# Performance work log

Hardware: AMD Instinct MI355X
Metric: run time of the kernel (lower is better)

## Reference

```python
import jax, jax.numpy as jnp
import numpy as np

B, N, D4 = 64, 2048, 4

def setup_inputs() -> dict:
    key = jax.random.key(0)
    k1, k2 = jax.random.split(key)
    p = jax.random.normal(k1, (B, N, D4), dtype=jnp.float32)
    q = jax.random.normal(k2, (B, N, D4), dtype=jnp.float32)
    return {"p": p, "q": q}

def reference(p, q):
    # loss_norm_choice='p3', im=False, take_sqrt=True, jet_features=False
    p3 = p[..., 1:]  # (B, N, 3) spatial momenta
    q3 = q[..., 1:]
    p_sq = jnp.sum(p3 * p3, axis=-1)                      # (B, N)
    q_sq = jnp.sum(q3 * q3, axis=-1)                      # (B, N)
    cross = jnp.einsum('bnd,bmd->bnm', p3, q3)            # (B, N, N)
    dist_sq = p_sq[:, :, None] + q_sq[:, None, :] - 2.0 * cross
    dist = jnp.sqrt(jnp.maximum(dist_sq, 0.0) + 1e-16)    # (B, N, N)
    min_pq = jnp.min(dist, axis=-1)                       # (B, N) nearest q for each p
    min_qp = jnp.min(dist, axis=-2)                       # (B, N) nearest p for each q
    return jnp.sum((min_pq + min_qp) * 0.5)
```

## Files before the change

kernel.cpp:

```cpp
#include <hip/hip_runtime.h>
#include <math.h>


typedef _Float16 half8 __attribute__((ext_vector_type(8)));
typedef float floatx16 __attribute__((ext_vector_type(16)));

constexpr int B_ = 64;
constexpr int N_ = 2048;
constexpr int NT = N_ / 32;
constexpr int BLOCK = 512;
constexpr int WPB = 8;
constexpr int BFRAGS = 2;
constexpr int IBLK = NT / (WPB * BFRAGS);
constexpr int NBLK = IBLK * B_ * 2;

__global__ __launch_bounds__(BLOCK, 4) void chamfer_mfma_kernel(
    const float* __restrict__ p, const float* __restrict__ q,
    float* __restrict__ partials)
{
    __shared__ half8 Aarr[NT * 64];
    __shared__ float wsum[WPB];

    const int dir = blockIdx.z;
    const int b   = blockIdx.y;
    const float4* rowsA = (const float4*)((dir == 0 ? q : p) + (size_t)b * N_ * 4);
    const float4* colsB = (const float4*)((dir == 0 ? p : q) + (size_t)b * N_ * 4);

    for (int j = threadIdx.x; j < N_; j += BLOCK) {
        float4 v = rowsA[j];
        _Float16 x = (_Float16)v.y, y = (_Float16)v.z, z = (_Float16)v.w;
        float xf = (float)x, yf = (float)y, zf = (float)z;
        float sq = fmaf(xf, xf, fmaf(yf, yf, zf * zf));
        half8 lo;
        lo[0] = x; lo[1] = y; lo[2] = z; lo[3] = (_Float16)1.0f;
        lo[4] = (_Float16)(-0.5f * sq);
        lo[5] = (_Float16)0.0f; lo[6] = (_Float16)0.0f; lo[7] = (_Float16)0.0f;
        half8 zero8;
#pragma unroll
        for (int e = 0; e < 8; ++e) zero8[e] = (_Float16)0.0f;
        const int tile = j >> 5, r = j & 31;
        Aarr[tile * 64 + r]      = lo;
        Aarr[tile * 64 + 32 + r] = zero8;
    }

    const int lane = threadIdx.x & 63;
    const int wid  = threadIdx.x >> 6;
    const int W    = blockIdx.x * WPB + wid;
    half8 bf[BFRAGS];
#pragma unroll
    for (int t = 0; t < BFRAGS; ++t) {
        float4 v = colsB[(W * BFRAGS + t) * 32 + (lane & 31)];
        _Float16 x = (_Float16)v.y, y = (_Float16)v.z, z = (_Float16)v.w;
        float xf = (float)x, yf = (float)y, zf = (float)z;
        float sq = fmaf(xf, xf, fmaf(yf, yf, zf * zf));
#pragma unroll
        for (int e = 0; e < 8; ++e) bf[t][e] = (_Float16)0.0f;
        if (lane < 32) {
            bf[t][0] = x; bf[t][1] = y; bf[t][2] = z;
            bf[t][3] = (_Float16)(-0.5f * sq);
            bf[t][4] = (_Float16)1.0f;
        }
    }
    __syncthreads();

    floatx16 zero;
#pragma unroll
    for (int i = 0; i < 16; ++i) zero[i] = 0.0f;

    float cmx0 = -3.4e38f, cmx1 = -3.4e38f;
#pragma unroll 4
    for (int J = 0; J < NT; ++J) {
        half8 afrag = Aarr[J * 64 + lane];
        floatx16 C0 = __builtin_amdgcn_mfma_f32_32x32x16_f16(afrag, bf[0], zero, 0, 0, 0);
        floatx16 C1 = __builtin_amdgcn_mfma_f32_32x32x16_f16(afrag, bf[1], zero, 0, 0, 0);
        {
            float m0 = fmaxf(fmaxf(C0[0],  C0[1]),  C0[2]);
            float m1 = fmaxf(fmaxf(C0[3],  C0[4]),  C0[5]);
            float m2 = fmaxf(fmaxf(C0[6],  C0[7]),  C0[8]);
            float m3 = fmaxf(fmaxf(C0[9],  C0[10]), C0[11]);
            float m4 = fmaxf(fmaxf(C0[12], C0[13]), C0[14]);
            float m5 = fmaxf(fmaxf(m0, m1), C0[15]);
            float m6 = fmaxf(fmaxf(m2, m3), m4);
            cmx0 = fmaxf(cmx0, fmaxf(m5, m6));
        }
        {
            float m0 = fmaxf(fmaxf(C1[0],  C1[1]),  C1[2]);
            float m1 = fmaxf(fmaxf(C1[3],  C1[4]),  C1[5]);
            float m2 = fmaxf(fmaxf(C1[6],  C1[7]),  C1[8]);
            float m3 = fmaxf(fmaxf(C1[9],  C1[10]), C1[11]);
            float m4 = fmaxf(fmaxf(C1[12], C1[13]), C1[14]);
            float m5 = fmaxf(fmaxf(m0, m1), C1[15]);
            float m6 = fmaxf(fmaxf(m2, m3), m4);
            cmx1 = fmaxf(cmx1, fmaxf(m5, m6));
        }
    }

    cmx0 = fmaxf(cmx0, __shfl_xor(cmx0, 32, 64));
    cmx1 = fmaxf(cmx1, __shfl_xor(cmx1, 32, 64));

    float local = sqrtf(fmaxf(-2.0f * cmx0, 0.0f) + 1e-16f)
                + sqrtf(fmaxf(-2.0f * cmx1, 0.0f) + 1e-16f);

#pragma unroll
    for (int off = 32; off > 0; off >>= 1)
        local += __shfl_xor(local, off, 64);

    if (lane == 0) wsum[wid] = local;
    __syncthreads();
    if (threadIdx.x == 0) {
        float s = 0.0f;
#pragma unroll
        for (int w = 0; w < WPB; ++w) s += wsum[w];
        partials[(blockIdx.z * B_ + blockIdx.y) * IBLK + blockIdx.x] = 0.25f * s;
    }
}

__global__ __launch_bounds__(NBLK) void chamfer_reduce_kernel(
    const float* __restrict__ partials, float* __restrict__ out)
{
    float v = partials[threadIdx.x];
#pragma unroll
    for (int off = 32; off > 0; off >>= 1)
        v += __shfl_xor(v, off, 64);

    __shared__ float wsum[NBLK / 64];
    if ((threadIdx.x & 63) == 0) wsum[threadIdx.x >> 6] = v;
    __syncthreads();
    if (threadIdx.x == 0) {
        float s = 0.0f;
#pragma unroll
        for (int w = 0; w < NBLK / 64; ++w) s += wsum[w];
        out[0] = s;
    }
}

extern "C" void kernel_launch(void* const* d_in, const int* in_sizes, int n_in,
                              void* d_out, int out_size, void* d_ws, size_t ws_size,
                              hipStream_t stream) {
    const float* p = (const float*)d_in[0];
    const float* q = (const float*)d_in[1];
    float* out = (float*)d_out;
    float* partials = (float*)d_ws;

    dim3 grid(IBLK, B_, 2);
    chamfer_mfma_kernel<<<grid, BLOCK, 0, stream>>>(p, q, partials);
    chamfer_reduce_kernel<<<1, NBLK, 0, stream>>>(partials, out);
}
```

Baseline: 23.56 us.

## Halve LDS staging with two-phase A tiles and one B fragment per wave

Blocks drop to 256 threads, and each wave now holds a single B fragment, so the grid grows to 16x64x2 blocks. The row operand is staged into LDS in two halves with compact 32-entry tiles, and lanes 32-63 feed zeros in registers instead of reading stored zero padding. This cuts LDS footprint and staging writes so more blocks can be resident. In exchange, every block reloads and converts the full A set, so total global reads and conversion work per MFMA roughly double, and an extra barrier phase is added. The reduce kernel becomes a 512-thread strided sum because there are now more partials.

```diff
diff --git a/kernel.cpp b/kernel.cpp
--- a/kernel.cpp
+++ b/kernel.cpp
@@ -8,17 +8,19 @@
 constexpr int B_ = 64;
 constexpr int N_ = 2048;
 constexpr int NT = N_ / 32;
-constexpr int BLOCK = 512;
-constexpr int WPB = 8;
-constexpr int BFRAGS = 2;
+constexpr int HT = NT / 2;
+constexpr int BLOCK = 256;
+constexpr int WPB = 4;
+constexpr int BFRAGS = 1;
 constexpr int IBLK = NT / (WPB * BFRAGS);
 constexpr int NBLK = IBLK * B_ * 2;
+constexpr int RBLOCK = 512;
 
-__global__ __launch_bounds__(BLOCK, 4) void chamfer_mfma_kernel(
+__global__ __launch_bounds__(BLOCK, 8) void chamfer_mfma_kernel(
     const float* __restrict__ p, const float* __restrict__ q,
     float* __restrict__ partials)
 {
-    __shared__ half8 Aarr[NT * 64];
+    __shared__ half8 Aarr[HT * 32];
     __shared__ float wsum[WPB];
 
     const int dir = blockIdx.z;
@@ -26,80 +28,70 @@
     const float4* rowsA = (const float4*)((dir == 0 ? q : p) + (size_t)b * N_ * 4);
     const float4* colsB = (const float4*)((dir == 0 ? p : q) + (size_t)b * N_ * 4);
 
-    for (int j = threadIdx.x; j < N_; j += BLOCK) {
-        float4 v = rowsA[j];
-        _Float16 x = (_Float16)v.y, y = (_Float16)v.z, z = (_Float16)v.w;
-        float xf = (float)x, yf = (float)y, zf = (float)z;
-        float sq = fmaf(xf, xf, fmaf(yf, yf, zf * zf));
-        half8 lo;
-        lo[0] = x; lo[1] = y; lo[2] = z; lo[3] = (_Float16)1.0f;
-        lo[4] = (_Float16)(-0.5f * sq);
-        lo[5] = (_Float16)0.0f; lo[6] = (_Float16)0.0f; lo[7] = (_Float16)0.0f;
-        half8 zero8;
-#pragma unroll
-        for (int e = 0; e < 8; ++e) zero8[e] = (_Float16)0.0f;
-        const int tile = j >> 5, r = j & 31;
-        Aarr[tile * 64 + r]      = lo;
-        Aarr[tile * 64 + 32 + r] = zero8;
-    }
-
     const int lane = threadIdx.x & 63;
     const int wid  = threadIdx.x >> 6;
-    const int W    = blockIdx.x * WPB + wid;
-    half8 bf[BFRAGS];
-#pragma unroll
-    for (int t = 0; t < BFRAGS; ++t) {
-        float4 v = colsB[(W * BFRAGS + t) * 32 + (lane & 31)];
+
+    half8 bf;
+    {
+        float4 v = colsB[(blockIdx.x * WPB + wid) * 32 + (lane & 31)];
         _Float16 x = (_Float16)v.y, y = (_Float16)v.z, z = (_Float16)v.w;
         float xf = (float)x, yf = (float)y, zf = (float)z;
         float sq = fmaf(xf, xf, fmaf(yf, yf, zf * zf));
 #pragma unroll
-        for (int e = 0; e < 8; ++e) bf[t][e] = (_Float16)0.0f;
+        for (int e = 0; e < 8; ++e) bf[e] = (_Float16)0.0f;
         if (lane < 32) {
-            bf[t][0] = x; bf[t][1] = y; bf[t][2] = z;
-            bf[t][3] = (_Float16)(-0.5f * sq);
-            bf[t][4] = (_Float16)1.0f;
+            bf[0] = x; bf[1] = y; bf[2] = z;
+            bf[3] = (_Float16)(-0.5f * sq);
+            bf[4] = (_Float16)1.0f;
         }
     }
-    __syncthreads();
+
+    half8 zero8;
+#pragma unroll
+    for (int e = 0; e < 8; ++e) zero8[e] = (_Float16)0.0f;
 
     floatx16 zero;
 #pragma unroll
     for (int i = 0; i < 16; ++i) zero[i] = 0.0f;
 
-    float cmx0 = -3.4e38f, cmx1 = -3.4e38f;
+    float cmx = -3.4e38f;
+
+    for (int ph = 0; ph < 2; ++ph) {
+        __syncthreads();
+
+        for (int t = 0; t < N_ / 2; t += BLOCK) {
+            const int lj = t + threadIdx.x;
+            float4 v = rowsA[ph * (N_ / 2) + lj];
+            _Float16 x = (_Float16)v.y, y = (_Float16)v.z, z = (_Float16)v.w;
+            float xf = (float)x, yf = (float)y, zf = (float)z;
+            float sq = fmaf(xf, xf, fmaf(yf, yf, zf * zf));
+            half8 lo;
+            lo[0] = x; lo[1] = y; lo[2] = z; lo[3] = (_Float16)1.0f;
+            lo[4] = (_Float16)(-0.5f * sq);
+            lo[5] = (_Float16)0.0f; lo[6] = (_Float16)0.0f; lo[7] = (_Float16)0.0f;
+            Aarr[(lj >> 5) * 32 + (lj & 31)] = lo;
+        }
+        __syncthreads();
+
 #pragma unroll 4
-    for (int J = 0; J < NT; ++J) {
-        half8 afrag = Aarr[J * 64 + lane];
-        floatx16 C0 = __builtin_amdgcn_mfma_f32_32x32x16_f16(afrag, bf[0], zero, 0, 0, 0);
-        floatx16 C1 = __builtin_amdgcn_mfma_f32_32x32x16_f16(afrag, bf[1], zero, 0, 0, 0);
-        {
-            float m0 = fmaxf(fmaxf(C0[0],  C0[1]),  C0[2]);
-            float m1 = fmaxf(fmaxf(C0[3],  C0[4]),  C0[5]);
-            float m2 = fmaxf(fmaxf(C0[6],  C0[7]),  C0[8]);
-            float m3 = fmaxf(fmaxf(C0[9],  C0[10]), C0[11]);
-            float m4 = fmaxf(fmaxf(C0[12], C0[13]), C0[14]);
-            float m5 = fmaxf(fmaxf(m0, m1), C0[15]);
+        for (int J = 0; J < HT; ++J) {
+            half8 af = zero8;
+            if (lane < 32) af = Aarr[J * 32 + lane];
+            floatx16 C = __builtin_amdgcn_mfma_f32_32x32x16_f16(af, bf, zero, 0, 0, 0);
+            float m0 = fmaxf(fmaxf(C[0],  C[1]),  C[2]);
+            float m1 = fmaxf(fmaxf(C[3],  C[4]),  C[5]);
+            float m2 = fmaxf(fmaxf(C[6],  C[7]),  C[8]);
+            float m3 = fmaxf(fmaxf(C[9],  C[10]), C[11]);
+            float m4 = fmaxf(fmaxf(C[12], C[13]), C[14]);
+            float m5 = fmaxf(fmaxf(m0, m1), C[15]);
             float m6 = fmaxf(fmaxf(m2, m3), m4);
-            cmx0 = fmaxf(cmx0, fmaxf(m5, m6));
-        }
-        {
-            float m0 = fmaxf(fmaxf(C1[0],  C1[1]),  C1[2]);
-            float m1 = fmaxf(fmaxf(C1[3],  C1[4]),  C1[5]);
-            float m2 = fmaxf(fmaxf(C1[6],  C1[7]),  C1[8]);
-            float m3 = fmaxf(fmaxf(C1[9],  C1[10]), C1[11]);
-            float m4 = fmaxf(fmaxf(C1[12], C1[13]), C1[14]);
-            float m5 = fmaxf(fmaxf(m0, m1), C1[15]);
-            float m6 = fmaxf(fmaxf(m2, m3), m4);
-            cmx1 = fmaxf(cmx1, fmaxf(m5, m6));
+            cmx = fmaxf(cmx, fmaxf(m5, m6));
         }
     }
 
-    cmx0 = fmaxf(cmx0, __shfl_xor(cmx0, 32, 64));
-    cmx1 = fmaxf(cmx1, __shfl_xor(cmx1, 32, 64));
+    cmx = fmaxf(cmx, __shfl_xor(cmx, 32, 64));
 
-    float local = sqrtf(fmaxf(-2.0f * cmx0, 0.0f) + 1e-16f)
-                + sqrtf(fmaxf(-2.0f * cmx1, 0.0f) + 1e-16f);
+    float local = sqrtf(fmaxf(-2.0f * cmx, 0.0f) + 1e-16f);
 
 #pragma unroll
     for (int off = 32; off > 0; off >>= 1)
@@ -115,21 +107,25 @@
     }
 }
 
-__global__ __launch_bounds__(NBLK) void chamfer_reduce_kernel(
+__global__ __launch_bounds__(RBLOCK) void chamfer_reduce_kernel(
     const float* __restrict__ partials, float* __restrict__ out)
 {
-    float v = partials[threadIdx.x];
+    float v = 0.0f;
+#pragma unroll
+    for (int k = 0; k < NBLK / RBLOCK; ++k)
+        v += partials[k * RBLOCK + threadIdx.x];
+
 #pragma unroll
     for (int off = 32; off > 0; off >>= 1)
         v += __shfl_xor(v, off, 64);
 
-    __shared__ float wsum[NBLK / 64];
+    __shared__ float wsum[RBLOCK / 64];
     if ((threadIdx.x & 63) == 0) wsum[threadIdx.x >> 6] = v;
     __syncthreads();
     if (threadIdx.x == 0) {
         float s = 0.0f;
 #pragma unroll
-        for (int w = 0; w < NBLK / 64; ++w) s += wsum[w];
+        for (int w = 0; w < RBLOCK / 64; ++w) s += wsum[w];
         out[0] = s;
     }
 }
@@ -144,5 +140,5 @@
 
     dim3 grid(IBLK, B_, 2);
     chamfer_mfma_kernel<<<grid, BLOCK, 0, stream>>>(p, q, partials);
-    chamfer_reduce_kernel<<<1, NBLK, 0, stream>>>(partials, out);
+    chamfer_reduce_kernel<<<1, RBLOCK, 0, stream>>>(partials, out);
 }
```

Result: slower. 30.74 us (+30.5%).

## Pack two A tiles per MFMA fragment using split K halves

Applied to the files above, without the earlier changes.

The shared A array now stores rows contiguously, so lanes 32-63 carry a second 32-row tile in the upper K half instead of zero padding. B fragments are split into LO and HI variants that select one K half, so each A load feeds four MFMAs covering two tiles. This halves shared-memory footprint and LDS reads while keeping the MFMA count the same, and it drops the zero-padding stores. In exchange it needs twice as many B fragment registers.

```diff
diff --git a/kernel.cpp b/kernel.cpp
--- a/kernel.cpp
+++ b/kernel.cpp
@@ -8,17 +8,29 @@
 constexpr int B_ = 64;
 constexpr int N_ = 2048;
 constexpr int NT = N_ / 32;
+constexpr int NPAIR = NT / 2;
 constexpr int BLOCK = 512;
 constexpr int WPB = 8;
 constexpr int BFRAGS = 2;
 constexpr int IBLK = NT / (WPB * BFRAGS);
 constexpr int NBLK = IBLK * B_ * 2;
 
+__device__ __forceinline__ float tree16(const floatx16& C, float acc) {
+    float m0 = fmaxf(fmaxf(C[0],  C[1]),  C[2]);
+    float m1 = fmaxf(fmaxf(C[3],  C[4]),  C[5]);
+    float m2 = fmaxf(fmaxf(C[6],  C[7]),  C[8]);
+    float m3 = fmaxf(fmaxf(C[9],  C[10]), C[11]);
+    float m4 = fmaxf(fmaxf(C[12], C[13]), C[14]);
+    float m5 = fmaxf(fmaxf(m0, m1), C[15]);
+    float m6 = fmaxf(fmaxf(m2, m3), m4);
+    return fmaxf(acc, fmaxf(m5, m6));
+}
+
 __global__ __launch_bounds__(BLOCK, 4) void chamfer_mfma_kernel(
     const float* __restrict__ p, const float* __restrict__ q,
     float* __restrict__ partials)
 {
-    __shared__ half8 Aarr[NT * 64];
+    __shared__ half8 Aarr[N_];
     __shared__ float wsum[WPB];
 
     const int dir = blockIdx.z;
@@ -35,18 +47,13 @@
         lo[0] = x; lo[1] = y; lo[2] = z; lo[3] = (_Float16)1.0f;
         lo[4] = (_Float16)(-0.5f * sq);
         lo[5] = (_Float16)0.0f; lo[6] = (_Float16)0.0f; lo[7] = (_Float16)0.0f;
-        half8 zero8;
-#pragma unroll
-        for (int e = 0; e < 8; ++e) zero8[e] = (_Float16)0.0f;
-        const int tile = j >> 5, r = j & 31;
-        Aarr[tile * 64 + r]      = lo;
-        Aarr[tile * 64 + 32 + r] = zero8;
+        Aarr[j] = lo;
     }
 
     const int lane = threadIdx.x & 63;
     const int wid  = threadIdx.x >> 6;
     const int W    = blockIdx.x * WPB + wid;
-    half8 bf[BFRAGS];
+    half8 bfLO[BFRAGS], bfHI[BFRAGS];
 #pragma unroll
     for (int t = 0; t < BFRAGS; ++t) {
         float4 v = colsB[(W * BFRAGS + t) * 32 + (lane & 31)];
@@ -54,11 +61,15 @@
         float xf = (float)x, yf = (float)y, zf = (float)z;
         float sq = fmaf(xf, xf, fmaf(yf, yf, zf * zf));
 #pragma unroll
-        for (int e = 0; e < 8; ++e) bf[t][e] = (_Float16)0.0f;
+        for (int e = 0; e < 8; ++e) { bfLO[t][e] = (_Float16)0.0f; bfHI[t][e] = (_Float16)0.0f; }
         if (lane < 32) {
-            bf[t][0] = x; bf[t][1] = y; bf[t][2] = z;
-            bf[t][3] = (_Float16)(-0.5f * sq);
-            bf[t][4] = (_Float16)1.0f;
+            bfLO[t][0] = x; bfLO[t][1] = y; bfLO[t][2] = z;
+            bfLO[t][3] = (_Float16)(-0.5f * sq);
+            bfLO[t][4] = (_Float16)1.0f;
+        } else {
+            bfHI[t][0] = x; bfHI[t][1] = y; bfHI[t][2] = z;
+            bfHI[t][3] = (_Float16)(-0.5f * sq);
+            bfHI[t][4] = (_Float16)1.0f;
         }
     }
     __syncthreads();
@@ -68,31 +79,17 @@
     for (int i = 0; i < 16; ++i) zero[i] = 0.0f;
 
     float cmx0 = -3.4e38f, cmx1 = -3.4e38f;
-#pragma unroll 4
-    for (int J = 0; J < NT; ++J) {
-        half8 afrag = Aarr[J * 64 + lane];
-        floatx16 C0 = __builtin_amdgcn_mfma_f32_32x32x16_f16(afrag, bf[0], zero, 0, 0, 0);
-        floatx16 C1 = __builtin_amdgcn_mfma_f32_32x32x16_f16(afrag, bf[1], zero, 0, 0, 0);
-        {
-            float m0 = fmaxf(fmaxf(C0[0],  C0[1]),  C0[2]);
-            float m1 = fmaxf(fmaxf(C0[3],  C0[4]),  C0[5]);
-            float m2 = fmaxf(fmaxf(C0[6],  C0[7]),  C0[8]);
-            float m3 = fmaxf(fmaxf(C0[9],  C0[10]), C0[11]);
-            float m4 = fmaxf(fmaxf(C0[12], C0[13]), C0[14]);
-            float m5 = fmaxf(fmaxf(m0, m1), C0[15]);
-            float m6 = fmaxf(fmaxf(m2, m3), m4);
-            cmx0 = fmaxf(cmx0, fmaxf(m5, m6));
-        }
-        {
-            float m0 = fmaxf(fmaxf(C1[0],  C1[1]),  C1[2]);
-            float m1 = fmaxf(fmaxf(C1[3],  C1[4]),  C1[5]);
-            float m2 = fmaxf(fmaxf(C1[6],  C1[7]),  C1[8]);
-            float m3 = fmaxf(fmaxf(C1[9],  C1[10]), C1[11]);
-            float m4 = fmaxf(fmaxf(C1[12], C1[13]), C1[14]);
-            float m5 = fmaxf(fmaxf(m0, m1), C1[15]);
-            float m6 = fmaxf(fmaxf(m2, m3), m4);
-            cmx1 = fmaxf(cmx1, fmaxf(m5, m6));
-        }
+#pragma unroll 2
+    for (int T = 0; T < NPAIR; ++T) {
+        half8 af = Aarr[T * 64 + lane];
+        floatx16 C00 = __builtin_amdgcn_mfma_f32_32x32x16_f16(af, bfLO[0], zero, 0, 0, 0);
+        floatx16 C01 = __builtin_amdgcn_mfma_f32_32x32x16_f16(af, bfLO[1], zero, 0, 0, 0);
+        floatx16 C10 = __builtin_amdgcn_mfma_f32_32x32x16_f16(af, bfHI[0], zero, 0, 0, 0);
+        floatx16 C11 = __builtin_amdgcn_mfma_f32_32x32x16_f16(af, bfHI[1], zero, 0, 0, 0);
+        cmx0 = tree16(C00, cmx0);
+        cmx1 = tree16(C01, cmx1);
+        cmx0 = tree16(C10, cmx0);
+        cmx1 = tree16(C11, cmx1);
     }
 
     cmx0 = fmaxf(cmx0, __shfl_xor(cmx0, 32, 64));
```

Result: no change. 23.20 us (-1.5%).
